# Optimization experiments

Hardware: AMD Instinct MI355X
Metric: run time of the kernel (lower is better)

## Reference

```python
import jax, jax.numpy as jnp
import numpy as np

N = 100000      # nodes
E = 1600000     # edges (avg degree 16)
F_IN = 128      # num_features
H = 128         # hidden_channels
OUT = 64        # out_channels


def _glorot(key, shape):
    lim = float(np.sqrt(6.0 / (shape[0] + shape[1])))
    return jax.random.uniform(key, shape, jnp.float32, -lim, lim)


def setup_inputs() -> dict:
    key = jax.random.key(0)
    ks = jax.random.split(key, 5)
    x = jax.random.normal(ks[0], (N, F_IN), jnp.float32)
    edge_index = jax.random.randint(ks[1], (2, E), 0, N, dtype=jnp.int64)
    W1 = _glorot(ks[2], (F_IN, H)); b1 = jnp.zeros((H,), jnp.float32)
    W2 = _glorot(ks[3], (H, H));    b2 = jnp.zeros((H,), jnp.float32)
    W3 = _glorot(ks[4], (H, OUT));  b3 = jnp.zeros((OUT,), jnp.float32)
    return {"x": x, "edge_index": edge_index,
            "W1": W1, "b1": b1, "W2": W2, "b2": b2, "W3": W3, "b3": b3}


def _gcn_conv(h, src, dst, norm, W, b, n):
    # PyG GCNConv: linear transform, then sym-normalized scatter aggregation, then bias
    h = h @ W                                   # [N, d_out]
    msg = h[src] * norm[:, None]                # gather + scale, [E+N, d_out]
    agg = jax.ops.segment_sum(msg, dst, num_segments=n)
    return agg + b


def reference(x, edge_index, W1, b1, W2, b2, W3, b3):
    n = x.shape[0]
    # add self-loops (GCNConv default add_self_loops=True)
    loop = jnp.arange(n, dtype=edge_index.dtype)
    src = jnp.concatenate([edge_index[0], loop])
    dst = jnp.concatenate([edge_index[1], loop])
    # symmetric normalization deg^-1/2[src] * deg^-1/2[dst]
    deg = jax.ops.segment_sum(jnp.ones_like(dst, x.dtype), dst, num_segments=n)
    dinv = jnp.where(deg > 0, jax.lax.rsqrt(deg), 0.0)
    norm = dinv[src] * dinv[dst]

    h = jax.nn.relu(_gcn_conv(x, src, dst, norm, W1, b1, n))  # dropout p=0 -> no-op
    h = jax.nn.relu(_gcn_conv(h, src, dst, norm, W2, b2, n))
    h = _gcn_conv(h, src, dst, norm, W3, b3, n)
    return jax.nn.log_softmax(h, axis=1)
```

## Files before the change

### kernel.cpp

```cpp
#include <hip/hip_runtime.h>
#include <stdint.h>
#include <math.h>

#define FIN 128

typedef __attribute__((ext_vector_type(8))) short short8v;
typedef __attribute__((ext_vector_type(4))) float float4v;
typedef __attribute__((ext_vector_type(2))) float float2v;

__device__ __forceinline__ float2 bf2_to_f2(uint32_t u) {
    union { uint32_t i; float f; } a, b;
    a.i = (u & 0xFFFFu) << 16;
    b.i = u & 0xFFFF0000u;
    return make_float2(a.f, b.f);
}
__device__ __forceinline__ uint32_t f2_to_bf2(float x, float y) {
    union { float f; uint32_t i; } a, b;
    a.f = x; b.f = y;
    uint32_t ax = a.i + 0x7FFF + ((a.i >> 16) & 1);
    uint32_t by = b.i + 0x7FFF + ((b.i >> 16) & 1);
    return (ax >> 16) | (by & 0xFFFF0000u);
}
__device__ __forceinline__ unsigned short f_to_bf(float x) {
    union { float f; uint32_t i; } a;
    a.f = x;
    uint32_t u = a.i + 0x7FFF + ((a.i >> 16) & 1);
    return (unsigned short)(u >> 16);
}
__device__ __forceinline__ void acc8_fma(float* acc, uint4 v, float w) {
    float2 f;
    f = bf2_to_f2(v.x); acc[0] = fmaf(w, f.x, acc[0]); acc[1] = fmaf(w, f.y, acc[1]);
    f = bf2_to_f2(v.y); acc[2] = fmaf(w, f.x, acc[2]); acc[3] = fmaf(w, f.y, acc[3]);
    f = bf2_to_f2(v.z); acc[4] = fmaf(w, f.x, acc[4]); acc[5] = fmaf(w, f.y, acc[5]);
    f = bf2_to_f2(v.w); acc[6] = fmaf(w, f.x, acc[6]); acc[7] = fmaf(w, f.y, acc[7]);
}
__device__ __forceinline__ void acc16_fp8_fma(float* acc, uint4 v, float w) {
    uint32_t us[4] = {v.x, v.y, v.z, v.w};
#pragma unroll
    for (int q = 0; q < 4; ++q) {
        float2v f0 = __builtin_amdgcn_cvt_pk_f32_fp8(us[q], false);
        float2v f1 = __builtin_amdgcn_cvt_pk_f32_fp8(us[q], true);
        acc[q * 4 + 0] = fmaf(w, f0.x, acc[q * 4 + 0]);
        acc[q * 4 + 1] = fmaf(w, f0.y, acc[q * 4 + 1]);
        acc[q * 4 + 2] = fmaf(w, f1.x, acc[q * 4 + 2]);
        acc[q * 4 + 3] = fmaf(w, f1.y, acc[q * 4 + 3]);
    }
}

__device__ __forceinline__ int edge_at(const void* ei, long long idx, int is32) {
    return is32 ? ((const int*)ei)[idx] : (int)((const long long*)ei)[idx];
}

#define SP_CHUNK 4096
__global__ __launch_bounds__(256) void splitA_kernel(const void* __restrict__ ei,
                                                     int* __restrict__ gCnt,
                                                     uint2* __restrict__ buf1,
                                                     int E, int capS) {
    __shared__ int hist[16];
    __shared__ int gbase[16];
    __shared__ int lflag;
    int t = threadIdx.x;
    if (t < 16) hist[t] = 0;
    if (t == 0) lflag = 0;
    long long base = (long long)blockIdx.x * SP_CHUNK;
    __syncthreads();
    {
        long long e = base + t;
        if (e < E && ((const int*)ei)[2 * e + 1] != 0) atomicOr(&lflag, 1);
    }
    __syncthreads();
    int is32 = lflag;
    uint32_t lrec[16], rs[16], rd[16];
#pragma unroll
    for (int j = 0; j < 16; ++j) {
        long long e = base + t + j * 256;
        if (e < E) {
            int s = edge_at(ei, e, is32);
            int d = edge_at(ei, (long long)E + e, is32);
            int b = d >> 13;
            int lofs = atomicAdd(&hist[b], 1);
            lrec[j] = ((uint32_t)lofs << 4) | (uint32_t)b;
            rs[j] = (uint32_t)s;
            rd[j] = (uint32_t)d;
        } else
            lrec[j] = 0xFFFFFFFFu;
    }
    __syncthreads();
    if (t < 16) gbase[t] = atomicAdd(&gCnt[t], hist[t]);
    __syncthreads();
#pragma unroll
    for (int j = 0; j < 16; ++j) {
        if (lrec[j] != 0xFFFFFFFFu) {
            int b = lrec[j] & 15;
            int pos = gbase[b] + (int)(lrec[j] >> 4);
            if (pos < capS) buf1[(size_t)b * capS + pos] = make_uint2(rs[j], rd[j]);
        }
    }
}

__global__ __launch_bounds__(256) void splitB_kernel(const int* __restrict__ gCnt,
                                                     const uint2* __restrict__ buf1,
                                                     int* __restrict__ cnt2,
                                                     uint32_t* __restrict__ buf2,
                                                     int capS, int cap2, int NB) {
    __shared__ int hist[128];
    __shared__ int gbase[128];
    int t = threadIdx.x;
    int s = blockIdx.y;
    if (t < 128) hist[t] = 0;
    __syncthreads();
    int m = gCnt[s];
    if (m > capS) m = capS;
    long long base = (long long)blockIdx.x * SP_CHUNK;
    uint32_t lrec[16], r32[16];
#pragma unroll
    for (int j = 0; j < 16; ++j) {
        long long i = base + t + j * 256;
        if (i < m) {
            uint2 r = buf1[(size_t)s * capS + i];
            int d = (int)r.y;
            int sub = (d >> 6) & 127;
            int lofs = atomicAdd(&hist[sub], 1);
            lrec[j] = ((uint32_t)lofs << 7) | (uint32_t)sub;
            r32[j] = (r.x << 6) | (uint32_t)(d & 63);
        } else
            lrec[j] = 0xFFFFFFFFu;
    }
    __syncthreads();
    if (t < 128) {
        int g = s * 128 + t;
        gbase[t] = (g < NB) ? atomicAdd(&cnt2[g], hist[t]) : 0;
    }
    __syncthreads();
#pragma unroll
    for (int j = 0; j < 16; ++j) {
        if (lrec[j] != 0xFFFFFFFFu) {
            int sub = lrec[j] & 127;
            int pos = gbase[sub] + (int)(lrec[j] >> 7);
            if (pos < cap2) buf2[(size_t)(s * 128 + sub) * cap2 + pos] = r32[j];
        }
    }
}

__global__ __launch_bounds__(256) void binB_kernel(const int* __restrict__ cnt2,
                                                   const uint32_t* __restrict__ buf2,
                                                   int* __restrict__ cnt,
                                                   float* __restrict__ dinv,
                                                   int n, int cap2) {
    __shared__ int h[64];
    int bin = blockIdx.x;
    int t = threadIdx.x;
    if (t < 64) h[t] = 0;
    __syncthreads();
    int m = cnt2[bin];
    if (m > cap2) m = cap2;
    const uint32_t* buf = buf2 + (size_t)bin * cap2;
    for (int i = t; i < m; i += 256) atomicAdd(&h[buf[i] & 63], 1);
    __syncthreads();
    if (t < 64) {
        int node = bin * 64 + t;
        if (node < n) {
            cnt[node] = h[t];
            dinv[node] = rsqrtf((float)h[t] + 1.0f);
        }
    }
}

__global__ __launch_bounds__(1024) void binScan_kernel(const int* __restrict__ cnt2,
                                                       int* __restrict__ binBase,
                                                       int NB, int cap2) {
    __shared__ int sm[1024];
    int t = threadIdx.x;
    int K = (NB + 1023) / 1024;
    int s = 0;
    for (int i = 0; i < K; ++i) {
        int idx = t * K + i;
        if (idx < NB) s += min(cnt2[idx], cap2);
    }
    sm[t] = s;
    __syncthreads();
    for (int off = 1; off < 1024; off <<= 1) {
        int v = 0;
        if (t >= off) v = sm[t - off];
        __syncthreads();
        sm[t] += v;
        __syncthreads();
    }
    int base = (t == 0) ? 0 : sm[t - 1];
    for (int i = 0; i < K; ++i) {
        int idx = t * K + i;
        if (idx < NB) {
            binBase[idx] = base;
            base += min(cnt2[idx], cap2);
        }
    }
}

__global__ __launch_bounds__(256) void binC_kernel(const int* __restrict__ cnt2,
                                                   const uint32_t* __restrict__ buf2,
                                                   const int* __restrict__ binBase,
                                                   const int* __restrict__ cnt,
                                                   int* __restrict__ rowend,
                                                   int* __restrict__ col, int n, int cap2) {
    __shared__ int rowst[64];
    __shared__ int cur[64];
    __shared__ int sc[64];
    int bin = blockIdx.x;
    int t = threadIdx.x;
    int c = 0;
    if (t < 64) {
        int node = bin * 64 + t;
        c = (node < n) ? cnt[node] : 0;
        sc[t] = c;
        cur[t] = 0;
    }
    __syncthreads();
    for (int off = 1; off < 64; off <<= 1) {
        int v = 0;
        if (t < 64 && t >= off) v = sc[t - off];
        __syncthreads();
        if (t < 64) sc[t] += v;
        __syncthreads();
    }
    if (t < 64) {
        int node = bin * 64 + t;
        int rs = binBase[bin] + sc[t] - c;
        rowst[t] = rs;
        if (node < n) rowend[node] = rs + c;
    }
    __syncthreads();
    int m = cnt2[bin];
    if (m > cap2) m = cap2;
    const uint32_t* buf = buf2 + (size_t)bin * cap2;
    for (int i = t; i < m; i += 256) {
        uint32_t rec = buf[i];
        int d6 = rec & 63;
        int off = atomicAdd(&cur[d6], 1);
        col[rowst[d6] + off] = (int)(rec >> 6);
    }
}

__global__ __launch_bounds__(256) void wconv_all(const float* __restrict__ W1,
                                                 const float* __restrict__ W2,
                                                 const float* __restrict__ W3,
                                                 unsigned short* __restrict__ Wf1,
                                                 unsigned short* __restrict__ Wf2,
                                                 unsigned short* __restrict__ Wf3) {
    int idx = blockIdx.x * 256 + threadIdx.x;
    const float* W;
    unsigned short* Wf;
    int NCOL, base;
    if (idx < 2048)      { W = W1; Wf = Wf1; NCOL = 128; base = idx; }
    else if (idx < 4096) { W = W2; Wf = Wf2; NCOL = 128; base = idx - 2048; }
    else if (idx < 5120) { W = W3; Wf = Wf3; NCOL = 64;  base = idx - 4096; }
    else return;
    int f = base >> 6, l = base & 63;
    int ct = f >> 2, ks = f & 3;
    int nn = ct * 16 + (l & 15);
    int k0 = ks * 32 + (l >> 4) * 8;
    uint32_t pk[4];
#pragma unroll
    for (int j = 0; j < 4; ++j) {
        float a = W[(size_t)(k0 + 2 * j) * NCOL + nn];
        float b = W[(size_t)(k0 + 2 * j + 1) * NCOL + nn];
        pk[j] = f2_to_bf2(a, b);
    }
    uint4 v = make_uint4(pk[0], pk[1], pk[2], pk[3]);
    ((uint4*)Wf)[base] = v;
}

template <int NCOL, int A_FP32, int OUT_FP8>
__global__ __launch_bounds__(256) void gemm_mfma(const void* __restrict__ Av,
                                                 const unsigned short* __restrict__ Wf,
                                                 const float* __restrict__ dinv,
                                                 void* __restrict__ Cv, int n) {
    __shared__ unsigned short lds[NCOL * 128];
    const int t = threadIdx.x;
    for (int i = t; i < NCOL * 16; i += 256)
        ((uint4*)lds)[i] = ((const uint4*)Wf)[i];
    __syncthreads();

    const int wave = t >> 6, lane = t & 63;
    const int row0 = blockIdx.x * 64 + wave * 16;
    const int m = lane & 15, quad = lane >> 4;
    int arow = row0 + m;
    if (arow >= n) arow = n - 1;

    short8v a[4];
    if (A_FP32) {
        const float* A = (const float*)Av;
#pragma unroll
        for (int ks = 0; ks < 4; ++ks) {
            float4 lo = *(const float4*)(A + (size_t)arow * 128 + ks * 32 + quad * 8);
            float4 hi = *(const float4*)(A + (size_t)arow * 128 + ks * 32 + quad * 8 + 4);
            union { short8v v; uint32_t u[4]; } pk;
            pk.u[0] = f2_to_bf2(lo.x, lo.y);
            pk.u[1] = f2_to_bf2(lo.z, lo.w);
            pk.u[2] = f2_to_bf2(hi.x, hi.y);
            pk.u[3] = f2_to_bf2(hi.z, hi.w);
            a[ks] = pk.v;
        }
    } else {
        const unsigned short* A = (const unsigned short*)Av;
#pragma unroll
        for (int ks = 0; ks < 4; ++ks)
            a[ks] = *(const short8v*)(A + (size_t)arow * 128 + ks * 32 + quad * 8);
    }

    const int cr0 = row0 + quad * 4;
    float ds[4];
#pragma unroll
    for (int r = 0; r < 4; ++r) {
        int gr = cr0 + r;
        ds[r] = (gr < n) ? dinv[gr] : 0.0f;
    }
#pragma unroll
    for (int ct = 0; ct < NCOL / 16; ++ct) {
        float4v acc = {0.0f, 0.0f, 0.0f, 0.0f};
#pragma unroll
        for (int ks = 0; ks < 4; ++ks) {
            int f = ct * 4 + ks;
            short8v b = *(const short8v*)(lds + ((size_t)(f * 64 + lane)) * 8);
            acc = __builtin_amdgcn_mfma_f32_16x16x32_bf16(a[ks], b, acc, 0, 0, 0);
        }
#pragma unroll
        for (int r = 0; r < 4; ++r) {
            int gr = cr0 + r;
            if (gr < n) {
                float val = acc[r] * ds[r];
                if (OUT_FP8) {
                    int u = __builtin_amdgcn_cvt_pk_fp8_f32(val, val, 0, false);
                    ((unsigned char*)Cv)[(size_t)gr * NCOL + ct * 16 + m] =
                        (unsigned char)(u & 0xFF);
                } else {
                    ((unsigned short*)Cv)[(size_t)gr * NCOL + ct * 16 + m] = f_to_bf(val);
                }
            }
        }
    }
}

__global__ __launch_bounds__(256) void agg_relu_128_fp8(
        const uint32_t* __restrict__ T8, const int* __restrict__ rowend,
        const int* __restrict__ cnt, const int* __restrict__ col,
        const float* __restrict__ dinv, const float* __restrict__ bias,
        uint32_t* __restrict__ outHb, int n) {
    int wid = blockIdx.x * 4 + (threadIdx.x >> 6);
    int lane = threadIdx.x & 63;
    int sel = lane >> 5, slot = (lane >> 3) & 3, j = lane & 7;
    int nodeA = wid * 2;
    int node = nodeA + sel;
    if (nodeA >= n) return;
    bool valid = node < n;
    int nd = valid ? node : nodeA;
    int end = rowend[nd];
    int start = end - cnt[nd];
    if (!valid) start = end;

    float acc[16];
#pragma unroll
    for (int k = 0; k < 16; ++k) acc[k] = 0.0f;
    if (slot == 0 && valid) {
        uint4 v = *(const uint4*)(T8 + (size_t)node * 32 + j * 4);
        acc16_fp8_fma(acc, v, 1.0f);
    }
    int deg = end - start;
    int degM = max(deg, __shfl_xor(deg, 32, 64));
    int p = start + slot;
    for (int it = 0; it < degM; it += 8) {
        int e0 = p, e1 = p + 4;
        float w0 = e0 < end ? 1.0f : 0.0f;
        float w1 = e1 < end ? 1.0f : 0.0f;
        int c0 = min(e0, end - 1); c0 = max(c0, 0);
        int c1 = min(e1, end - 1); c1 = max(c1, 0);
        int s0 = col[c0], s1 = col[c1];
        uint4 v0 = *(const uint4*)(T8 + (size_t)s0 * 32 + j * 4);
        uint4 v1 = *(const uint4*)(T8 + (size_t)s1 * 32 + j * 4);
        acc16_fp8_fma(acc, v0, w0);
        acc16_fp8_fma(acc, v1, w1);
        p += 8;
    }
#pragma unroll
    for (int k = 0; k < 16; ++k) {
        acc[k] += __shfl_xor(acc[k], 8, 64);
        acc[k] += __shfl_xor(acc[k], 16, 64);
    }
    if (slot == 0 && valid) {
        float di = dinv[node];
        const float4* b4 = (const float4*)bias;
        float r[16];
#pragma unroll
        for (int q = 0; q < 4; ++q) {
            float4 bb = b4[j * 4 + q];
            r[q * 4 + 0] = fmaxf(di * acc[q * 4 + 0] + bb.x, 0.0f);
            r[q * 4 + 1] = fmaxf(di * acc[q * 4 + 1] + bb.y, 0.0f);
            r[q * 4 + 2] = fmaxf(di * acc[q * 4 + 2] + bb.z, 0.0f);
            r[q * 4 + 3] = fmaxf(di * acc[q * 4 + 3] + bb.w, 0.0f);
        }
        uint4 o0, o1;
        o0.x = f2_to_bf2(r[0], r[1]);   o0.y = f2_to_bf2(r[2], r[3]);
        o0.z = f2_to_bf2(r[4], r[5]);   o0.w = f2_to_bf2(r[6], r[7]);
        o1.x = f2_to_bf2(r[8], r[9]);   o1.y = f2_to_bf2(r[10], r[11]);
        o1.z = f2_to_bf2(r[12], r[13]); o1.w = f2_to_bf2(r[14], r[15]);
        *(uint4*)(outHb + (size_t)node * 64 + j * 8) = o0;
        *(uint4*)(outHb + (size_t)node * 64 + j * 8 + 4) = o1;
    }
}

__global__ __launch_bounds__(256) void agg_lsm_64_w2(
        const unsigned short* __restrict__ T, const int* __restrict__ rowend,
        const int* __restrict__ cnt, const int* __restrict__ col,
        const float* __restrict__ dinv, const float* __restrict__ bias,
        float* __restrict__ out, int n) {
    int wid = blockIdx.x * 4 + (threadIdx.x >> 6);
    int lane = threadIdx.x & 63;
    int sel = lane >> 5, slot = (lane >> 3) & 3, j = lane & 7;
    int node = wid * 2 + sel;
    int nodeA = wid * 2;
    if (nodeA >= n) return;
    bool valid = node < n;
    int nd = valid ? node : nodeA;
    int end = rowend[nd];
    int start = end - cnt[nd];
    if (!valid) start = end;

    float acc[8];
#pragma unroll
    for (int k = 0; k < 8; ++k) acc[k] = 0.0f;
    if (slot == 0 && valid) {
        uint4 v = *(const uint4*)(T + (size_t)node * 64 + j * 8);
        acc8_fma(acc, v, 1.0f);
    }
    int deg = end - start;
    int degM = max(deg, __shfl_xor(deg, 32, 64));
    int p = start + slot;
    for (int it = 0; it < degM; it += 8) {
        int e0 = p, e1 = p + 4;
        float w0 = e0 < end ? 1.0f : 0.0f;
        float w1 = e1 < end ? 1.0f : 0.0f;
        int c0 = min(e0, end - 1); c0 = max(c0, 0);
        int c1 = min(e1, end - 1); c1 = max(c1, 0);
        int s0 = col[c0], s1 = col[c1];
        uint4 v0 = *(const uint4*)(T + (size_t)s0 * 64 + j * 8);
        uint4 v1 = *(const uint4*)(T + (size_t)s1 * 64 + j * 8);
        acc8_fma(acc, v0, w0);
        acc8_fma(acc, v1, w1);
        p += 8;
    }
#pragma unroll
    for (int k = 0; k < 8; ++k) {
        acc[k] += __shfl_xor(acc[k], 8, 64);
        acc[k] += __shfl_xor(acc[k], 16, 64);
    }
    float di = dinv[nd];
    const float4* b4 = (const float4*)bias;
    float4 ba = b4[j * 2], bb = b4[j * 2 + 1];
    float r[8];
    r[0] = di * acc[0] + ba.x; r[1] = di * acc[1] + ba.y;
    r[2] = di * acc[2] + ba.z; r[3] = di * acc[3] + ba.w;
    r[4] = di * acc[4] + bb.x; r[5] = di * acc[5] + bb.y;
    r[6] = di * acc[6] + bb.z; r[7] = di * acc[7] + bb.w;
    float m = r[0];
#pragma unroll
    for (int k = 1; k < 8; ++k) m = fmaxf(m, r[k]);
    m = fmaxf(m, __shfl_xor(m, 1, 64));
    m = fmaxf(m, __shfl_xor(m, 2, 64));
    m = fmaxf(m, __shfl_xor(m, 4, 64));
    float ss = 0.0f;
#pragma unroll
    for (int k = 0; k < 8; ++k) ss += expf(r[k] - m);
    ss += __shfl_xor(ss, 1, 64);
    ss += __shfl_xor(ss, 2, 64);
    ss += __shfl_xor(ss, 4, 64);
    float lg = m + logf(ss);
    if (slot == 0 && valid) {
        float4 o0 = make_float4(r[0] - lg, r[1] - lg, r[2] - lg, r[3] - lg);
        float4 o1 = make_float4(r[4] - lg, r[5] - lg, r[6] - lg, r[7] - lg);
        *(float4*)(out + (size_t)node * 64 + j * 8) = o0;
        *(float4*)(out + (size_t)node * 64 + j * 8 + 4) = o1;
    }
}

extern "C" void kernel_launch(void* const* d_in, const int* in_sizes, int n_in,
                              void* d_out, int out_size, void* d_ws, size_t ws_size,
                              hipStream_t stream) {
    const float* x  = (const float*)d_in[0];
    const void*  ei = d_in[1];
    const float* W1 = (const float*)d_in[2];
    const float* b1 = (const float*)d_in[3];
    const float* W2 = (const float*)d_in[4];
    const float* b2 = (const float*)d_in[5];
    const float* W3 = (const float*)d_in[6];
    const float* b3 = (const float*)d_in[7];
    float* out = (float*)d_out;

    const int n = in_sizes[0] / FIN;
    const int E = in_sizes[1] / 2;

    char* p = (char*)d_ws;
    auto carve = [&](size_t bytes) {
        char* q = p;
        p += (bytes + 255) & ~(size_t)255;
        return q;
    };
    const int NB = (n + 63) / 64;
    const int NS = (n + 8191) / 8192;

    int*   cnt     = (int*)carve((size_t)n * 4);
    int*   rowend  = (int*)carve((size_t)n * 4);
    float* dinv    = (float*)carve((size_t)n * 4);
    int*   colb    = (int*)carve((size_t)E * 4);
    int*   gCnt    = (int*)carve((size_t)(16 + NB) * 4);
    int*   cnt2    = gCnt + 16;
    int*   binBase = (int*)carve((size_t)NB * 4);
    size_t Tbytes = (size_t)n * 128;
    size_t Hbytes = (size_t)n * 128 * 2;
    char*  TH = carve(Tbytes + Hbytes);
    void*  T  = (void*)TH;
    unsigned short* Hb = (unsigned short*)(TH + Tbytes);
    unsigned short* Wf1 = (unsigned short*)carve(128 * 128 * 2);
    unsigned short* Wf2 = (unsigned short*)carve(128 * 128 * 2);
    unsigned short* Wf3 = (unsigned short*)carve(128 * 64 * 2);

    long long meanS = (long long)E * 8192 / n;
    int capS = (int)(meanS + 8 * (long long)sqrt((double)meanS) + 1024);
    capS = (capS + 15) & ~15;
    long long mean2 = (long long)E * 64 / n;
    int cap2 = (int)(mean2 + 8 * (long long)sqrt((double)mean2) + 64);
    cap2 = (cap2 + 15) & ~15;
    size_t buf1B = ((size_t)NS * capS * 8 + 255) & ~(size_t)255;
    uint2*    buf1 = (uint2*)TH;
    uint32_t* buf2 = (uint32_t*)(TH + buf1B);
    size_t avail2 = (Tbytes + Hbytes > buf1B) ? (Tbytes + Hbytes - buf1B) : 0;
    size_t maxc2 = avail2 / ((size_t)NB * 4);
    if ((size_t)cap2 > maxc2) cap2 = (int)maxc2;

    hipMemsetAsync(gCnt, 0, (size_t)(16 + NB) * 4, stream);

    const int gagg2 = ((n + 1) / 2 + 3) / 4;
    const int ggemm = (n + 63) / 64;
    const int gsplitA = (E + SP_CHUNK - 1) / SP_CHUNK;
    const int gsplitBx = (capS + SP_CHUNK - 1) / SP_CHUNK;

    splitA_kernel<<<gsplitA, 256, 0, stream>>>(ei, gCnt, buf1, E, capS);
    splitB_kernel<<<dim3(gsplitBx, NS), 256, 0, stream>>>(gCnt, buf1, cnt2, buf2, capS,
                                                          cap2, NB);
    binB_kernel<<<NB, 256, 0, stream>>>(cnt2, buf2, cnt, dinv, n, cap2);
    binScan_kernel<<<1, 1024, 0, stream>>>(cnt2, binBase, NB, cap2);
    binC_kernel<<<NB, 256, 0, stream>>>(cnt2, buf2, binBase, cnt, rowend, colb, n, cap2);
    wconv_all<<<20, 256, 0, stream>>>(W1, W2, W3, Wf1, Wf2, Wf3);

    gemm_mfma<128, 1, 1><<<ggemm, 256, 0, stream>>>(x, Wf1, dinv, T, n);
    agg_relu_128_fp8<<<gagg2, 256, 0, stream>>>((const uint32_t*)T, rowend, cnt, colb,
                                                dinv, b1, (uint32_t*)Hb, n);
    gemm_mfma<128, 0, 1><<<ggemm, 256, 0, stream>>>(Hb, Wf2, dinv, T, n);
    agg_relu_128_fp8<<<gagg2, 256, 0, stream>>>((const uint32_t*)T, rowend, cnt, colb,
                                                dinv, b2, (uint32_t*)Hb, n);
    gemm_mfma<64, 0, 0><<<ggemm, 256, 0, stream>>>(Hb, Wf3, dinv, T, n);
    agg_lsm_64_w2<<<gagg2, 256, 0, stream>>>((const unsigned short*)T, rowend, cnt,
                                             colb, dinv, b3, out, n);
}
```

Baseline: 305.5 us.

## Fuse CSR build kernels, pack edge records, use fp8 for final layer aggregation

```diff
diff --git a/kernel.cpp b/kernel.cpp
--- a/kernel.cpp
+++ b/kernel.cpp
@@ -27,23 +27,12 @@
     uint32_t u = a.i + 0x7FFF + ((a.i >> 16) & 1);
     return (unsigned short)(u >> 16);
 }
-__device__ __forceinline__ void acc8_fma(float* acc, uint4 v, float w) {
-    float2 f;
-    f = bf2_to_f2(v.x); acc[0] = fmaf(w, f.x, acc[0]); acc[1] = fmaf(w, f.y, acc[1]);
-    f = bf2_to_f2(v.y); acc[2] = fmaf(w, f.x, acc[2]); acc[3] = fmaf(w, f.y, acc[3]);
-    f = bf2_to_f2(v.z); acc[4] = fmaf(w, f.x, acc[4]); acc[5] = fmaf(w, f.y, acc[5]);
-    f = bf2_to_f2(v.w); acc[6] = fmaf(w, f.x, acc[6]); acc[7] = fmaf(w, f.y, acc[7]);
-}
-__device__ __forceinline__ void acc16_fp8_fma(float* acc, uint4 v, float w) {
+__device__ __forceinline__ void acc16_fp8_pk(float2v* acc2, uint4 v) {
     uint32_t us[4] = {v.x, v.y, v.z, v.w};
 #pragma unroll
     for (int q = 0; q < 4; ++q) {
-        float2v f0 = __builtin_amdgcn_cvt_pk_f32_fp8(us[q], false);
-        float2v f1 = __builtin_amdgcn_cvt_pk_f32_fp8(us[q], true);
-        acc[q * 4 + 0] = fmaf(w, f0.x, acc[q * 4 + 0]);
-        acc[q * 4 + 1] = fmaf(w, f0.y, acc[q * 4 + 1]);
-        acc[q * 4 + 2] = fmaf(w, f1.x, acc[q * 4 + 2]);
-        acc[q * 4 + 3] = fmaf(w, f1.y, acc[q * 4 + 3]);
+        acc2[q * 2 + 0] += __builtin_amdgcn_cvt_pk_f32_fp8(us[q], false);
+        acc2[q * 2 + 1] += __builtin_amdgcn_cvt_pk_f32_fp8(us[q], true);
     }
 }
 
@@ -54,7 +43,7 @@
 #define SP_CHUNK 4096
 __global__ __launch_bounds__(256) void splitA_kernel(const void* __restrict__ ei,
                                                      int* __restrict__ gCnt,
-                                                     uint2* __restrict__ buf1,
+                                                     uint32_t* __restrict__ buf1,
                                                      int E, int capS) {
     __shared__ int hist[16];
     __shared__ int gbase[16];
@@ -70,7 +59,7 @@
     }
     __syncthreads();
     int is32 = lflag;
-    uint32_t lrec[16], rs[16], rd[16];
+    uint32_t lrec[16], rec[16];
 #pragma unroll
     for (int j = 0; j < 16; ++j) {
         long long e = base + t + j * 256;
@@ -80,8 +69,7 @@
             int b = d >> 13;
             int lofs = atomicAdd(&hist[b], 1);
             lrec[j] = ((uint32_t)lofs << 4) | (uint32_t)b;
-            rs[j] = (uint32_t)s;
-            rd[j] = (uint32_t)d;
+            rec[j] = ((uint32_t)s << 13) | (uint32_t)(d & 8191);
         } else
             lrec[j] = 0xFFFFFFFFu;
     }
@@ -93,13 +81,13 @@
         if (lrec[j] != 0xFFFFFFFFu) {
             int b = lrec[j] & 15;
             int pos = gbase[b] + (int)(lrec[j] >> 4);
-            if (pos < capS) buf1[(size_t)b * capS + pos] = make_uint2(rs[j], rd[j]);
+            if (pos < capS) buf1[(size_t)b * capS + pos] = rec[j];
         }
     }
 }
 
 __global__ __launch_bounds__(256) void splitB_kernel(const int* __restrict__ gCnt,
-                                                     const uint2* __restrict__ buf1,
+                                                     const uint32_t* __restrict__ buf1,
                                                      int* __restrict__ cnt2,
                                                      uint32_t* __restrict__ buf2,
                                                      int capS, int cap2, int NB) {
@@ -117,12 +105,12 @@
     for (int j = 0; j < 16; ++j) {
         long long i = base + t + j * 256;
         if (i < m) {
-            uint2 r = buf1[(size_t)s * capS + i];
-            int d = (int)r.y;
-            int sub = (d >> 6) & 127;
+            uint32_t r = buf1[(size_t)s * capS + i];
+            int d13 = (int)(r & 8191u);
+            int sub = d13 >> 6;
             int lofs = atomicAdd(&hist[sub], 1);
             lrec[j] = ((uint32_t)lofs << 7) | (uint32_t)sub;
-            r32[j] = (r.x << 6) | (uint32_t)(d & 63);
+            r32[j] = ((r >> 13) << 6) | (uint32_t)(d13 & 63);
         } else
             lrec[j] = 0xFFFFFFFFu;
     }
@@ -142,78 +130,28 @@
     }
 }
 
-__global__ __launch_bounds__(256) void binB_kernel(const int* __restrict__ cnt2,
-                                                   const uint32_t* __restrict__ buf2,
-                                                   int* __restrict__ cnt,
-                                                   float* __restrict__ dinv,
-                                                   int n, int cap2) {
+__global__ __launch_bounds__(256) void binBC_kernel(const int* __restrict__ cnt2,
+                                                    const uint32_t* __restrict__ buf2,
+                                                    int* __restrict__ cnt,
+                                                    float* __restrict__ dinv,
+                                                    int* __restrict__ rowend,
+                                                    int* __restrict__ col,
+                                                    int n, int cap2) {
     __shared__ int h[64];
-    int bin = blockIdx.x;
-    int t = threadIdx.x;
-    if (t < 64) h[t] = 0;
-    __syncthreads();
-    int m = cnt2[bin];
-    if (m > cap2) m = cap2;
-    const uint32_t* buf = buf2 + (size_t)bin * cap2;
-    for (int i = t; i < m; i += 256) atomicAdd(&h[buf[i] & 63], 1);
-    __syncthreads();
-    if (t < 64) {
-        int node = bin * 64 + t;
-        if (node < n) {
-            cnt[node] = h[t];
-            dinv[node] = rsqrtf((float)h[t] + 1.0f);
-        }
-    }
-}
-
-__global__ __launch_bounds__(1024) void binScan_kernel(const int* __restrict__ cnt2,
-                                                       int* __restrict__ binBase,
-                                                       int NB, int cap2) {
-    __shared__ int sm[1024];
-    int t = threadIdx.x;
-    int K = (NB + 1023) / 1024;
-    int s = 0;
-    for (int i = 0; i < K; ++i) {
-        int idx = t * K + i;
-        if (idx < NB) s += min(cnt2[idx], cap2);
-    }
-    sm[t] = s;
-    __syncthreads();
-    for (int off = 1; off < 1024; off <<= 1) {
-        int v = 0;
-        if (t >= off) v = sm[t - off];
-        __syncthreads();
-        sm[t] += v;
-        __syncthreads();
-    }
-    int base = (t == 0) ? 0 : sm[t - 1];
-    for (int i = 0; i < K; ++i) {
-        int idx = t * K + i;
-        if (idx < NB) {
-            binBase[idx] = base;
-            base += min(cnt2[idx], cap2);
-        }
-    }
-}
-
-__global__ __launch_bounds__(256) void binC_kernel(const int* __restrict__ cnt2,
-                                                   const uint32_t* __restrict__ buf2,
-                                                   const int* __restrict__ binBase,
-                                                   const int* __restrict__ cnt,
-                                                   int* __restrict__ rowend,
-                                                   int* __restrict__ col, int n, int cap2) {
     __shared__ int rowst[64];
     __shared__ int cur[64];
     __shared__ int sc[64];
     int bin = blockIdx.x;
     int t = threadIdx.x;
+    if (t < 64) { h[t] = 0; cur[t] = 0; }
+    __syncthreads();
+    int m = cnt2[bin];
+    if (m > cap2) m = cap2;
+    const uint32_t* buf = buf2 + (size_t)bin * cap2;
+    for (int i = t; i < m; i += 256) atomicAdd(&h[buf[i] & 63], 1);
+    __syncthreads();
     int c = 0;
-    if (t < 64) {
-        int node = bin * 64 + t;
-        c = (node < n) ? cnt[node] : 0;
-        sc[t] = c;
-        cur[t] = 0;
-    }
+    if (t < 64) { c = h[t]; sc[t] = c; }
     __syncthreads();
     for (int off = 1; off < 64; off <<= 1) {
         int v = 0;
@@ -224,14 +162,15 @@
     }
     if (t < 64) {
         int node = bin * 64 + t;
-        int rs = binBase[bin] + sc[t] - c;
-        rowst[t] = rs;
-        if (node < n) rowend[node] = rs + c;
-    }
-    __syncthreads();
-    int m = cnt2[bin];
-    if (m > cap2) m = cap2;
-    const uint32_t* buf = buf2 + (size_t)bin * cap2;
+        int base = bin * cap2;
+        rowst[t] = base + sc[t] - c;
+        if (node < n) {
+            cnt[node] = c;
+            dinv[node] = rsqrtf((float)c + 1.0f);
+            rowend[node] = base + sc[t];
+        }
+    }
+    __syncthreads();
     for (int i = t; i < m; i += 256) {
         uint32_t rec = buf[i];
         int d6 = rec & 63;
@@ -357,29 +296,32 @@
     int start = end - cnt[nd];
     if (!valid) start = end;
 
-    float acc[16];
-#pragma unroll
-    for (int k = 0; k < 16; ++k) acc[k] = 0.0f;
+    float2v acc2[8];
+#pragma unroll
+    for (int k = 0; k < 8; ++k) acc2[k] = (float2v){0.0f, 0.0f};
     if (slot == 0 && valid) {
         uint4 v = *(const uint4*)(T8 + (size_t)node * 32 + j * 4);
-        acc16_fp8_fma(acc, v, 1.0f);
+        acc16_fp8_pk(acc2, v);
     }
     int deg = end - start;
     int degM = max(deg, __shfl_xor(deg, 32, 64));
     int p = start + slot;
+    const uint4 Z = make_uint4(0, 0, 0, 0);
     for (int it = 0; it < degM; it += 8) {
         int e0 = p, e1 = p + 4;
-        float w0 = e0 < end ? 1.0f : 0.0f;
-        float w1 = e1 < end ? 1.0f : 0.0f;
+        bool k0 = e0 < end, k1 = e1 < end;
         int c0 = min(e0, end - 1); c0 = max(c0, 0);
         int c1 = min(e1, end - 1); c1 = max(c1, 0);
         int s0 = col[c0], s1 = col[c1];
         uint4 v0 = *(const uint4*)(T8 + (size_t)s0 * 32 + j * 4);
         uint4 v1 = *(const uint4*)(T8 + (size_t)s1 * 32 + j * 4);
-        acc16_fp8_fma(acc, v0, w0);
-        acc16_fp8_fma(acc, v1, w1);
+        if (!k0) v0 = Z;
+        if (!k1) v1 = Z;
+        acc16_fp8_pk(acc2, v0);
+        acc16_fp8_pk(acc2, v1);
         p += 8;
     }
+    float* acc = (float*)acc2;
 #pragma unroll
     for (int k = 0; k < 16; ++k) {
         acc[k] += __shfl_xor(acc[k], 8, 64);
@@ -407,16 +349,16 @@
     }
 }
 
-__global__ __launch_bounds__(256) void agg_lsm_64_w2(
-        const unsigned short* __restrict__ T, const int* __restrict__ rowend,
+__global__ __launch_bounds__(256) void agg_lsm_64_fp8(
+        const uint32_t* __restrict__ T8, const int* __restrict__ rowend,
         const int* __restrict__ cnt, const int* __restrict__ col,
         const float* __restrict__ dinv, const float* __restrict__ bias,
         float* __restrict__ out, int n) {
     int wid = blockIdx.x * 4 + (threadIdx.x >> 6);
     int lane = threadIdx.x & 63;
-    int sel = lane >> 5, slot = (lane >> 3) & 3, j = lane & 7;
-    int node = wid * 2 + sel;
+    int sel = lane >> 5, slot = (lane >> 2) & 7, j = lane & 3;
     int nodeA = wid * 2;
+    int node = nodeA + sel;
     if (nodeA >= n) return;
     bool valid = node < n;
     int nd = valid ? node : nodeA;
@@ -424,60 +366,67 @@
     int start = end - cnt[nd];
     if (!valid) start = end;
 
-    float acc[8];
-#pragma unroll
-    for (int k = 0; k < 8; ++k) acc[k] = 0.0f;
+    float2v acc2[8];
+#pragma unroll
+    for (int k = 0; k < 8; ++k) acc2[k] = (float2v){0.0f, 0.0f};
     if (slot == 0 && valid) {
-        uint4 v = *(const uint4*)(T + (size_t)node * 64 + j * 8);
-        acc8_fma(acc, v, 1.0f);
+        uint4 v = *(const uint4*)(T8 + (size_t)node * 16 + j * 4);
+        acc16_fp8_pk(acc2, v);
     }
     int deg = end - start;
     int degM = max(deg, __shfl_xor(deg, 32, 64));
     int p = start + slot;
-    for (int it = 0; it < degM; it += 8) {
-        int e0 = p, e1 = p + 4;
-        float w0 = e0 < end ? 1.0f : 0.0f;
-        float w1 = e1 < end ? 1.0f : 0.0f;
+    const uint4 Z = make_uint4(0, 0, 0, 0);
+    for (int it = 0; it < degM; it += 16) {
+        int e0 = p, e1 = p + 8;
+        bool k0 = e0 < end, k1 = e1 < end;
         int c0 = min(e0, end - 1); c0 = max(c0, 0);
         int c1 = min(e1, end - 1); c1 = max(c1, 0);
         int s0 = col[c0], s1 = col[c1];
-        uint4 v0 = *(const uint4*)(T + (size_t)s0 * 64 + j * 8);
-        uint4 v1 = *(const uint4*)(T + (size_t)s1 * 64 + j * 8);
-        acc8_fma(acc, v0, w0);
-        acc8_fma(acc, v1, w1);
-        p += 8;
-    }
-#pragma unroll
-    for (int k = 0; k < 8; ++k) {
+        uint4 v0 = *(const uint4*)(T8 + (size_t)s0 * 16 + j * 4);
+        uint4 v1 = *(const uint4*)(T8 + (size_t)s1 * 16 + j * 4);
+        if (!k0) v0 = Z;
+        if (!k1) v1 = Z;
+        acc16_fp8_pk(acc2, v0);
+        acc16_fp8_pk(acc2, v1);
+        p += 16;
+    }
+    float* acc = (float*)acc2;
+#pragma unroll
+    for (int k = 0; k < 16; ++k) {
+        acc[k] += __shfl_xor(acc[k], 4, 64);
         acc[k] += __shfl_xor(acc[k], 8, 64);
         acc[k] += __shfl_xor(acc[k], 16, 64);
     }
     float di = dinv[nd];
     const float4* b4 = (const float4*)bias;
-    float4 ba = b4[j * 2], bb = b4[j * 2 + 1];
-    float r[8];
-    r[0] = di * acc[0] + ba.x; r[1] = di * acc[1] + ba.y;
-    r[2] = di * acc[2] + ba.z; r[3] = di * acc[3] + ba.w;
-    r[4] = di * acc[4] + bb.x; r[5] = di * acc[5] + bb.y;
-    r[6] = di * acc[6] + bb.z; r[7] = di * acc[7] + bb.w;
+    float r[16];
+#pragma unroll
+    for (int q = 0; q < 4; ++q) {
+        float4 bb = b4[j * 4 + q];
+        r[q * 4 + 0] = di * acc[q * 4 + 0] + bb.x;
+        r[q * 4 + 1] = di * acc[q * 4 + 1] + bb.y;
+        r[q * 4 + 2] = di * acc[q * 4 + 2] + bb.z;
+        r[q * 4 + 3] = di * acc[q * 4 + 3] + bb.w;
+    }
     float m = r[0];
 #pragma unroll
-    for (int k = 1; k < 8; ++k) m = fmaxf(m, r[k]);
+    for (int k = 1; k < 16; ++k) m = fmaxf(m, r[k]);
     m = fmaxf(m, __shfl_xor(m, 1, 64));
     m = fmaxf(m, __shfl_xor(m, 2, 64));
-    m = fmaxf(m, __shfl_xor(m, 4, 64));
     float ss = 0.0f;
 #pragma unroll
-    for (int k = 0; k < 8; ++k) ss += expf(r[k] - m);
+    for (int k = 0; k < 16; ++k) ss += expf(r[k] - m);
     ss += __shfl_xor(ss, 1, 64);
     ss += __shfl_xor(ss, 2, 64);
-    ss += __shfl_xor(ss, 4, 64);
     float lg = m + logf(ss);
     if (slot == 0 && valid) {
-        float4 o0 = make_float4(r[0] - lg, r[1] - lg, r[2] - lg, r[3] - lg);
-        float4 o1 = make_float4(r[4] - lg, r[5] - lg, r[6] - lg, r[7] - lg);
-        *(float4*)(out + (size_t)node * 64 + j * 8) = o0;
-        *(float4*)(out + (size_t)node * 64 + j * 8 + 4) = o1;
+#pragma unroll
+        for (int q = 0; q < 4; ++q) {
+            float4 o = make_float4(r[q * 4 + 0] - lg, r[q * 4 + 1] - lg,
+                                   r[q * 4 + 2] - lg, r[q * 4 + 3] - lg);
+            *(float4*)(out + (size_t)node * 64 + j * 16 + q * 4) = o;
+        }
     }
 }
 
@@ -506,13 +455,19 @@
     const int NB = (n + 63) / 64;
     const int NS = (n + 8191) / 8192;
 
+    long long meanS = (long long)E * 8192 / n;
+    int capS = (int)(meanS + 8 * (long long)sqrt((double)meanS) + 1024);
+    capS = (capS + 15) & ~15;
+    long long mean2 = (long long)E * 64 / n;
+    int cap2 = (int)(mean2 + 8 * (long long)sqrt((double)mean2) + 64);
+    cap2 = (cap2 + 15) & ~15;
+
     int*   cnt     = (int*)carve((size_t)n * 4);
     int*   rowend  = (int*)carve((size_t)n * 4);
     float* dinv    = (float*)carve((size_t)n * 4);
-    int*   colb    = (int*)carve((size_t)E * 4);
+    int*   colb    = (int*)carve((size_t)NB * cap2 * 4);
     int*   gCnt    = (int*)carve((size_t)(16 + NB) * 4);
     int*   cnt2    = gCnt + 16;
-    int*   binBase = (int*)carve((size_t)NB * 4);
     size_t Tbytes = (size_t)n * 128;
     size_t Hbytes = (size_t)n * 128 * 2;
     char*  TH = carve(Tbytes + Hbytes);
@@ -522,14 +477,8 @@
     unsigned short* Wf2 = (unsigned short*)carve(128 * 128 * 2);
     unsigned short* Wf3 = (unsigned short*)carve(128 * 64 * 2);
 
-    long long meanS = (long long)E * 8192 / n;
-    int capS = (int)(meanS + 8 * (long long)sqrt((double)meanS) + 1024);
-    capS = (capS + 15) & ~15;
-    long long mean2 = (long long)E * 64 / n;
-    int cap2 = (int)(mean2 + 8 * (long long)sqrt((double)mean2) + 64);
-    cap2 = (cap2 + 15) & ~15;
-    size_t buf1B = ((size_t)NS * capS * 8 + 255) & ~(size_t)255;
-    uint2*    buf1 = (uint2*)TH;
+    size_t buf1B = ((size_t)NS * capS * 4 + 255) & ~(size_t)255;
+    uint32_t* buf1 = (uint32_t*)TH;
     uint32_t* buf2 = (uint32_t*)(TH + buf1B);
     size_t avail2 = (Tbytes + Hbytes > buf1B) ? (Tbytes + Hbytes - buf1B) : 0;
     size_t maxc2 = avail2 / ((size_t)NB * 4);
@@ -545,9 +494,7 @@
     splitA_kernel<<<gsplitA, 256, 0, stream>>>(ei, gCnt, buf1, E, capS);
     splitB_kernel<<<dim3(gsplitBx, NS), 256, 0, stream>>>(gCnt, buf1, cnt2, buf2, capS,
                                                           cap2, NB);
-    binB_kernel<<<NB, 256, 0, stream>>>(cnt2, buf2, cnt, dinv, n, cap2);
-    binScan_kernel<<<1, 1024, 0, stream>>>(cnt2, binBase, NB, cap2);
-    binC_kernel<<<NB, 256, 0, stream>>>(cnt2, buf2, binBase, cnt, rowend, colb, n, cap2);
+    binBC_kernel<<<NB, 256, 0, stream>>>(cnt2, buf2, cnt, dinv, rowend, colb, n, cap2);
     wconv_all<<<20, 256, 0, stream>>>(W1, W2, W3, Wf1, Wf2, Wf3);
 
     gemm_mfma<128, 1, 1><<<ggemm, 256, 0, stream>>>(x, Wf1, dinv, T, n);
@@ -556,7 +503,7 @@
     gemm_mfma<128, 0, 1><<<ggemm, 256, 0, stream>>>(Hb, Wf2, dinv, T, n);
     agg_relu_128_fp8<<<gagg2, 256, 0, stream>>>((const uint32_t*)T, rowend, cnt, colb,
                                                 dinv, b2, (uint32_t*)Hb, n);
-    gemm_mfma<64, 0, 0><<<ggemm, 256, 0, stream>>>(Hb, Wf3, dinv, T, n);
-    agg_lsm_64_w2<<<gagg2, 256, 0, stream>>>((const unsigned short*)T, rowend, cnt,
-                                             colb, dinv, b3, out, n);
-}
+    gemm_mfma<64, 0, 1><<<ggemm, 256, 0, stream>>>(Hb, Wf3, dinv, T, n);
+    agg_lsm_64_fp8<<<gagg2, 256, 0, stream>>>((const uint32_t*)T, rowend, cnt, colb,
+                                              dinv, b3, out, n);
+}
```

After: 304.9 us. Within noise of the previous version (-0.2%).
